# Kernel tuning notes

Hardware: AMD Instinct MI355X
Metric: run time of the kernel (lower is better)

The kernel has to match this reference:

```python
import jax, jax.numpy as jnp
import numpy as np

B, L, S, HKV, G, D = 2, 4096, 128, 4, 16, 128
TOPK, BLOCK_SIZE, WINDOW = 16, 32, 64


def setup_inputs() -> dict:
    key = jax.random.key(0)
    kq, kk = jax.random.split(key)
    Q = jax.random.normal(kq, (B, L, HKV, G, D), dtype=jnp.bfloat16)
    K = jax.random.normal(kk, (B, S, HKV, D), dtype=jnp.bfloat16)
    return {"Q": Q, "K": K}


def reference(Q, K):
    """Fused top-k max pooling (NSA block selection).
    1) scores = Q @ K^T per group (no scaling for selection)
    2) max-pool over groups, causal-mask compressed blocks
    3) per-(b, tq, kv-head) top-k block indices; invalid (-inf) -> -1
    4) sort indices ascending (-1 treated as S, placed at end)
    5) recompute per-group scores for selected blocks, scaled by 1/sqrt(D);
       invalid slots -> -inf.
    Returns (out_scores [B,L,h,G,topk] fp32, indices [B,L,h,topk] int32).
    """
    Qf = Q.astype(jnp.float32)
    Kf = K.astype(jnp.float32)

    # [B, L, h, G, S] raw scores, then max over groups -> [B, L, h, S]
    scores = jnp.einsum('blhgd,bshd->blhgs', Qf, Kf)
    pooled = scores.max(axis=3)

    # causal mask in compressed-block space: masked when ts >= (tq - W + 1)//block
    tq = jnp.arange(L)[:, None]
    ts = jnp.arange(S)[None, :]
    limit = (tq - WINDOW + 1) // BLOCK_SIZE  # floor div; same effect as kernel for ts>=0
    masked = ts >= limit                      # [L, S]
    pooled = jnp.where(masked[None, :, None, :], -jnp.inf, pooled)

    # top-k over compressed blocks
    vals, idx = jax.lax.top_k(pooled, TOPK)           # [B, L, h, TOPK]
    idx = jnp.where(jnp.isneginf(vals), -1, idx).astype(jnp.int32)

    # sort ascending, invalid (-1) keyed as S so they land at the end
    sort_key = jnp.where(idx < 0, S, idx)
    order = jnp.argsort(sort_key, axis=-1)
    idx_sorted = jnp.take_along_axis(idx, order, axis=-1)  # [B, L, h, TOPK]

    # gather selected K rows: Kf [B,S,h,D] -> [B,h,L,TOPK,D]
    safe_idx = jnp.maximum(idx_sorted, 0)
    Kbh = jnp.transpose(Kf, (0, 2, 1, 3))                  # [B, h, S, D]
    idx_bh = jnp.transpose(safe_idx, (0, 2, 1, 3))          # [B, h, L, TOPK]
    Ksel = jnp.take_along_axis(Kbh[:, :, None, :, :], idx_bh[..., None], axis=3)

    sm_scale = 1.0 / np.sqrt(D).astype(np.float32)
    out = jnp.einsum('blhgd,bhlkd->blhgk', Qf, Ksel) * sm_scale
    out = jnp.where((idx_sorted >= 0)[:, :, :, None, :], out, -jnp.inf)
    return out, idx_sorted
```

## Files before the change

kernel.cpp:

```cpp
#include <hip/hip_runtime.h>
#include <hip/hip_bf16.h>

#define B_    2
#define L_    4096
#define S_    128
#define HKV_  4
#define G_    16
#define D_    128
#define TOPK_ 16
#define BLKW_ 32
#define WIN_  64

typedef __attribute__((ext_vector_type(8))) __bf16 bf16x8;
typedef __attribute__((ext_vector_type(4))) float  f32x4;

__global__ __launch_bounds__(256) void nsa_topk_pool(
    const __hip_bfloat16* __restrict__ Qg,
    const __hip_bfloat16* __restrict__ Kg,
    float* __restrict__ out_sc,
    float* __restrict__ out_ix)
{
    __shared__ float sc_all[4][S_][G_ + 1];
    __shared__ int   six_all[4][TOPK_];

    const int wid  = threadIdx.x >> 6;
    const int lane = threadIdx.x & 63;
    const int c    = lane & 15;
    const int kg   = lane >> 4;

    const int task = blockIdx.x * 4 + wid;
    const int b    = task / (HKV_ * L_);
    const int r    = task % (HKV_ * L_);
    const int h    = r / L_;
    const int tq   = r % L_;

    float (*sc)[G_ + 1] = sc_all[wid];

    const __hip_bfloat16* Qp =
        Qg + ((((size_t)b * L_ + tq) * HKV_ + h) * G_ + c) * D_ + kg * 8;
    bf16x8 afr[4];
#pragma unroll
    for (int ks = 0; ks < 4; ++ks)
        afr[ks] = *reinterpret_cast<const bf16x8*>(Qp + ks * 32);

    const __hip_bfloat16* Kp =
        Kg + (((size_t)b * S_ + c) * HKV_ + h) * D_ + kg * 8;
    f32x4 acc[8];
#pragma unroll
    for (int t = 0; t < 8; ++t) acc[t] = (f32x4){0.f, 0.f, 0.f, 0.f};
#pragma unroll
    for (int ks = 0; ks < 4; ++ks) {
#pragma unroll
        for (int t = 0; t < 8; ++t) {
            bf16x8 bfr = *reinterpret_cast<const bf16x8*>(
                Kp + (size_t)t * 16 * (HKV_ * D_) + ks * 32);
            acc[t] = __builtin_amdgcn_mfma_f32_16x16x32_bf16(afr[ks], bfr, acc[t], 0, 0, 0);
        }
    }

#pragma unroll
    for (int t = 0; t < 8; ++t) {
#pragma unroll
        for (int rg = 0; rg < 4; ++rg)
            sc[c + 16 * t][kg * 4 + rg] = acc[t][rg];
    }
    __syncthreads();

    const float NEG_INF = -__builtin_inff();
    const int num   = tq - (WIN_ - 1);
    const int limit = (num >= 0) ? (num / BLKW_) : -((-num + BLKW_ - 1) / BLKW_);

    const int s0 = lane, s1 = lane + 64;
    float v0 = NEG_INF, v1 = NEG_INF;
    if (s0 < limit) {
        float m = sc[s0][0];
#pragma unroll
        for (int g = 1; g < G_; ++g) m = fmaxf(m, sc[s0][g]);
        v0 = m;
    }
    if (s1 < limit) {
        float m = sc[s1][0];
#pragma unroll
        for (int g = 1; g < G_; ++g) m = fmaxf(m, sc[s1][g]);
        v1 = m;
    }

    float wv[TOPK_]; int wi[TOPK_];
#pragma unroll
    for (int k = 0; k < TOPK_; ++k) {
        float bv; int bi;
        if (v0 >= v1) { bv = v0; bi = s0; } else { bv = v1; bi = s1; }
#pragma unroll
        for (int m = 1; m < 64; m <<= 1) {
            float ov = __shfl_xor(bv, m, 64);
            int   oi = __shfl_xor(bi, m, 64);
            if (ov > bv || (ov == bv && oi < bi)) { bv = ov; bi = oi; }
        }
        wv[k] = bv; wi[k] = bi;
        if (bi == s0) v0 = NEG_INF;
        if (bi == s1) v1 = NEG_INF;
    }

    int key[TOPK_];
#pragma unroll
    for (int k = 0; k < TOPK_; ++k)
        key[k] = (wv[k] == NEG_INF) ? (S_ + k) : wi[k];

    int my_sorted = -1;
#pragma unroll
    for (int k = 0; k < TOPK_; ++k) {
        int rank = 0;
#pragma unroll
        for (int j = 0; j < TOPK_; ++j) rank += (key[j] < key[k]);
        if (rank == lane) my_sorted = (key[k] >= S_) ? -1 : key[k];
    }

    const size_t obase = (((size_t)b * L_ + tq) * HKV_ + h);
    if (lane < TOPK_) {
        out_ix[obase * TOPK_ + lane] = (float)my_sorted;
        six_all[wid][lane] = my_sorted;
    }
    __syncthreads();

    const float SENTINEL = -1e30f;
    const float scale = 0.08838834764831845f;
    const int g  = lane >> 2;
    const int k0 = (lane & 3) * 4;
    f32x4 o;
#pragma unroll
    for (int j = 0; j < 4; ++j) {
        int si = six_all[wid][k0 + j];
        o[j] = (si >= 0) ? sc[si][g] * scale : SENTINEL;
    }
    *reinterpret_cast<f32x4*>(out_sc + (obase * G_ + g) * TOPK_ + k0) = o;
}

extern "C" void kernel_launch(void* const* d_in, const int* in_sizes, int n_in,
                              void* d_out, int out_size, void* d_ws, size_t ws_size,
                              hipStream_t stream) {
    const __hip_bfloat16* Q = (const __hip_bfloat16*)d_in[0];
    const __hip_bfloat16* K = (const __hip_bfloat16*)d_in[1];
    float* out_sc = (float*)d_out;
    float* out_ix = out_sc + (size_t)B_ * L_ * HKV_ * G_ * TOPK_;

    const int n_tasks = B_ * HKV_ * L_;
    dim3 grid(n_tasks / 4), block(256);
    nsa_topk_pool<<<grid, block, 0, stream>>>(Q, K, out_sc, out_ix);
}
```

Before: 435.6 us.

## Register max-pool, packed-key DPP top-k, bitmask sort, MFMA rescoring

Removes the per-wave shared-memory score table. Group max-pooling is now done in registers with cross-lane shuffles. Top-k packs each truncated float score and its block index into one unsigned key, so every round needs a single DPP row-max plus readlane reduction, and the loop exits early once no valid candidates remain. Sorting is replaced by ballot/mbcnt compaction over a selection mask, and the selected scores are recomputed with one extra MFMA per wave over gathered K rows instead of being read from LDS. This cuts LDS footprint and traffic and should raise occupancy. In exchange it adds extra K reads and truncates the low 7 mantissa bits in comparisons, which can change tie-breaking.

```diff
diff --git a/kernel.cpp b/kernel.cpp
--- a/kernel.cpp
+++ b/kernel.cpp
@@ -14,14 +14,20 @@
 typedef __attribute__((ext_vector_type(8))) __bf16 bf16x8;
 typedef __attribute__((ext_vector_type(4))) float  f32x4;
 
+__device__ __forceinline__ int mbcnt64(unsigned long long m) {
+    return __builtin_amdgcn_mbcnt_hi((unsigned)(m >> 32),
+           __builtin_amdgcn_mbcnt_lo((unsigned)(m & 0xFFFFFFFFull), 0));
+}
+
+__device__ __forceinline__ unsigned umax2(unsigned a, unsigned b) { return a > b ? a : b; }
+
 __global__ __launch_bounds__(256) void nsa_topk_pool(
     const __hip_bfloat16* __restrict__ Qg,
     const __hip_bfloat16* __restrict__ Kg,
     float* __restrict__ out_sc,
     float* __restrict__ out_ix)
 {
-    __shared__ float sc_all[4][S_][G_ + 1];
-    __shared__ int   six_all[4][TOPK_];
+    __shared__ int six_all[4][TOPK_];
 
     const int wid  = threadIdx.x >> 6;
     const int lane = threadIdx.x & 63;
@@ -29,12 +35,13 @@
     const int kg   = lane >> 4;
 
     const int task = blockIdx.x * 4 + wid;
-    const int b    = task / (HKV_ * L_);
-    const int r    = task % (HKV_ * L_);
-    const int h    = r / L_;
-    const int tq   = r % L_;
+    const int b    = task >> 14;
+    const int rrem = task & 16383;
+    const int h    = rrem >> 12;
+    const int tq   = rrem & 4095;
 
-    float (*sc)[G_ + 1] = sc_all[wid];
+    int* six = six_all[wid];
+    if (lane < TOPK_) six[lane] = -1;
 
     const __hip_bfloat16* Qp =
         Qg + ((((size_t)b * L_ + tq) * HKV_ + h) * G_ + c) * D_ + kg * 8;
@@ -58,81 +65,83 @@
         }
     }
 
+    float lmax[8];
+#pragma unroll
+    for (int t = 0; t < 8; ++t)
+        lmax[t] = fmaxf(fmaxf(acc[t][0], acc[t][1]), fmaxf(acc[t][2], acc[t][3]));
 #pragma unroll
     for (int t = 0; t < 8; ++t) {
-#pragma unroll
-        for (int rg = 0; rg < 4; ++rg)
-            sc[c + 16 * t][kg * 4 + rg] = acc[t][rg];
+        lmax[t] = fmaxf(lmax[t], __shfl_xor(lmax[t], 16, 64));
+        lmax[t] = fmaxf(lmax[t], __shfl_xor(lmax[t], 32, 64));
     }
+    const int tsel = lane >> 4;
+    float a01 = (tsel & 1) ? lmax[1] : lmax[0];
+    float a23 = (tsel & 1) ? lmax[3] : lmax[2];
+    float v0  = (tsel & 2) ? a23 : a01;
+    float b01 = (tsel & 1) ? lmax[5] : lmax[4];
+    float b23 = (tsel & 1) ? lmax[7] : lmax[6];
+    float v1  = (tsel & 2) ? b23 : b01;
+
+    const int num   = tq - (WIN_ - 1);
+    const int limit = (num >= 0) ? (num / BLKW_) : -((-num + BLKW_ - 1) / BLKW_);
+    int ib0 = __float_as_int(v0);
+    int ib1 = __float_as_int(v1);
+    unsigned m0 = (unsigned)ib0 ^ (unsigned)((ib0 >> 31) | 0x80000000);
+    unsigned m1 = (unsigned)ib1 ^ (unsigned)((ib1 >> 31) | 0x80000000);
+    unsigned c0 = (lane      < limit) ? ((m0 & 0xFFFFFF80u) | (unsigned)(127 - lane)) : 0u;
+    unsigned c1 = (lane + 64 < limit) ? ((m1 & 0xFFFFFF80u) | (unsigned)( 63 - lane)) : 0u;
+
+    bool p0 = false, p1 = false;
+    for (int k = 0; k < TOPK_; ++k) {
+        unsigned m = umax2(c0, c1);
+        m = umax2(m, (unsigned)__builtin_amdgcn_update_dpp(0, (int)m, 0x121, 0xF, 0xF, true));
+        m = umax2(m, (unsigned)__builtin_amdgcn_update_dpp(0, (int)m, 0x122, 0xF, 0xF, true));
+        m = umax2(m, (unsigned)__builtin_amdgcn_update_dpp(0, (int)m, 0x124, 0xF, 0xF, true));
+        m = umax2(m, (unsigned)__builtin_amdgcn_update_dpp(0, (int)m, 0x128, 0xF, 0xF, true));
+        unsigned w0 = (unsigned)__builtin_amdgcn_readlane((int)m, 0);
+        unsigned w1 = (unsigned)__builtin_amdgcn_readlane((int)m, 16);
+        unsigned w2 = (unsigned)__builtin_amdgcn_readlane((int)m, 32);
+        unsigned w3 = (unsigned)__builtin_amdgcn_readlane((int)m, 48);
+        unsigned wk = umax2(umax2(w0, w1), umax2(w2, w3));
+        if (wk < 128u) break;
+        bool h0 = (c0 == wk);
+        bool h1 = (c1 == wk);
+        p0 |= h0; p1 |= h1;
+        if (h0) c0 = 0u;
+        if (h1) c1 = 0u;
+    }
+
+    unsigned long long blo = __ballot(p0);
+    unsigned long long bhi = __ballot(p1);
+    const int nlo  = __popcll(blo);
+    const int pos0 = mbcnt64(blo);
+    const int pos1 = nlo + mbcnt64(bhi);
+
+    __syncthreads();
+    if (p0) six[pos0] = lane;
+    if (p1) six[pos1] = lane + 64;
     __syncthreads();
 
-    const float NEG_INF = -__builtin_inff();
-    const int num   = tq - (WIN_ - 1);
-    const int limit = (num >= 0) ? (num / BLKW_) : -((-num + BLKW_ - 1) / BLKW_);
+    const size_t obase = (((size_t)b * L_ + tq) * HKV_ + h);
+    if (lane < TOPK_)
+        out_ix[obase * TOPK_ + lane] = (float)six[lane];
 
-    const int s0 = lane, s1 = lane + 64;
-    float v0 = NEG_INF, v1 = NEG_INF;
-    if (s0 < limit) {
-        float m = sc[s0][0];
+    const int si_c = six[c];
+    const int rowp = si_c < 0 ? 0 : si_c;
+    const __hip_bfloat16* Kr =
+        Kg + (((size_t)b * S_ + rowp) * HKV_ + h) * D_ + kg * 8;
+    f32x4 o = (f32x4){0.f, 0.f, 0.f, 0.f};
 #pragma unroll
-        for (int g = 1; g < G_; ++g) m = fmaxf(m, sc[s0][g]);
-        v0 = m;
+    for (int ks = 0; ks < 4; ++ks) {
+        bf16x8 bfr = *reinterpret_cast<const bf16x8*>(Kr + ks * 32);
+        o = __builtin_amdgcn_mfma_f32_16x16x32_bf16(afr[ks], bfr, o, 0, 0, 0);
     }
-    if (s1 < limit) {
-        float m = sc[s1][0];
+    const float SENT  = -1e30f;
+    const float scale = 0.08838834764831845f;
+    float* outp = out_sc + obase * (G_ * TOPK_) + c;
 #pragma unroll
-        for (int g = 1; g < G_; ++g) m = fmaxf(m, sc[s1][g]);
-        v1 = m;
-    }
-
-    float wv[TOPK_]; int wi[TOPK_];
-#pragma unroll
-    for (int k = 0; k < TOPK_; ++k) {
-        float bv; int bi;
-        if (v0 >= v1) { bv = v0; bi = s0; } else { bv = v1; bi = s1; }
-#pragma unroll
-        for (int m = 1; m < 64; m <<= 1) {
-            float ov = __shfl_xor(bv, m, 64);
-            int   oi = __shfl_xor(bi, m, 64);
-            if (ov > bv || (ov == bv && oi < bi)) { bv = ov; bi = oi; }
-        }
-        wv[k] = bv; wi[k] = bi;
-        if (bi == s0) v0 = NEG_INF;
-        if (bi == s1) v1 = NEG_INF;
-    }
-
-    int key[TOPK_];
-#pragma unroll
-    for (int k = 0; k < TOPK_; ++k)
-        key[k] = (wv[k] == NEG_INF) ? (S_ + k) : wi[k];
-
-    int my_sorted = -1;
-#pragma unroll
-    for (int k = 0; k < TOPK_; ++k) {
-        int rank = 0;
-#pragma unroll
-        for (int j = 0; j < TOPK_; ++j) rank += (key[j] < key[k]);
-        if (rank == lane) my_sorted = (key[k] >= S_) ? -1 : key[k];
-    }
-
-    const size_t obase = (((size_t)b * L_ + tq) * HKV_ + h);
-    if (lane < TOPK_) {
-        out_ix[obase * TOPK_ + lane] = (float)my_sorted;
-        six_all[wid][lane] = my_sorted;
-    }
-    __syncthreads();
-
-    const float SENTINEL = -1e30f;
-    const float scale = 0.08838834764831845f;
-    const int g  = lane >> 2;
-    const int k0 = (lane & 3) * 4;
-    f32x4 o;
-#pragma unroll
-    for (int j = 0; j < 4; ++j) {
-        int si = six_all[wid][k0 + j];
-        o[j] = (si >= 0) ? sc[si][g] * scale : SENTINEL;
-    }
-    *reinterpret_cast<f32x4*>(out_sc + (obase * G_ + g) * TOPK_ + k0) = o;
+    for (int rg = 0; rg < 4; ++rg)
+        outp[(kg * 4 + rg) * TOPK_] = (si_c >= 0) ? o[rg] * scale : SENT;
 }
 
 extern "C" void kernel_launch(void* const* d_in, const int* in_sizes, int n_in,
```

Measured after the change: 433.8 us. No clear change (-0.4%).
